# Optimization experiments

Measured on AMD Instinct MI355X. Metric: run time of the kernel, lower is better.

## Reference

```python
import jax, jax.numpy as jnp
import numpy as np

K, R, A, F, T = 100000, 5, 8, 32, 96
ROTATION_DELTA = 1


def setup_inputs() -> dict:
    key = jax.random.key(0)
    k1, k2, k3, k4, k5, k6, k7 = jax.random.split(key, 7)
    # barycentric coordinates: last dim packs (vertex_index, weight)
    idx = jax.random.randint(k1, (K, R, A, 3), 0, K)
    w = jax.random.uniform(k2, (K, R, A, 3), dtype=jnp.float32)
    w = w / jnp.sum(w, axis=-1, keepdims=True)
    bary_coordinates = jnp.stack([idx.astype(jnp.float32), w], axis=-1)  # (K,R,A,3,2)
    mesh_signal = jax.random.normal(k3, (K, F), dtype=jnp.float32)
    # kernel from define_kernel_values (abstract): fixed prior interpolation weights (R,A,R,A)
    kernel = jax.random.normal(k4, (R, A, R, A), dtype=jnp.float32) * 0.1
    template_neighbor_weights = jax.random.normal(k5, (T, R, A, F), dtype=jnp.float32) * 0.05
    template_self_weights = jax.random.normal(k6, (T, 1, F), dtype=jnp.float32) * 0.05
    bias = jax.random.normal(k7, (T,), dtype=jnp.float32) * 0.01
    return {
        "mesh_signal": mesh_signal,
        "bary_coordinates": bary_coordinates,
        "kernel": kernel,
        "template_neighbor_weights": template_neighbor_weights,
        "template_self_weights": template_self_weights,
        "bias": bias,
    }


def reference(mesh_signal, bary_coordinates, kernel, template_neighbor_weights,
              template_self_weights, bias):
    # --- signal retrieval: barycentric gather + interpolation ---
    idx = bary_coordinates[..., 0].astype(jnp.int32)          # (K,R,A,3)
    bw = bary_coordinates[..., 1]                              # (K,R,A,3)
    gathered = mesh_signal[idx]                                # (K,R,A,3,F)
    interp = jnp.sum(bw[..., None] * gathered, axis=-2)        # (K,R,A,F)
    # --- prior kernel fold (include_prior=True) ---
    interp = jnp.einsum('raxy,kxyf->kraf', kernel, interp)     # (K,R,A,F)
    # --- center contribution ---
    conv_center = jnp.einsum('tef,kf->ket', template_self_weights, mesh_signal)  # (K,1,T)
    # --- per-rotation template fold (torch.range is end-inclusive -> A//delta + 1 rotations) ---
    orientations = list(range(0, A + 1, ROTATION_DELTA))
    conv_neighbor = jnp.stack(
        [jnp.einsum('traf,kraf->kt', template_neighbor_weights,
                    jnp.roll(interp, o, axis=2)) + bias
         for o in orientations],
        axis=1)                                                # (K,O,T)
    return jax.nn.relu(conv_center + conv_neighbor)            # (K,O,T)
```

## Files before the change

### kernel.cpp

```cpp
#include <hip/hip_runtime.h>
#include <hip/hip_bf16.h>
#include <stdint.h>


typedef __attribute__((ext_vector_type(8))) short short8;
typedef __attribute__((ext_vector_type(4))) short short4v;
typedef __attribute__((ext_vector_type(4))) float floatx4;
typedef __attribute__((ext_vector_type(2))) float fx2;

#define KPTS 100000
#define OUT_STRIDE 864
#define BM 64
#define THREADS 512

#define BARRIER() do {                              \
    __builtin_amdgcn_sched_barrier(0);              \
    asm volatile("s_waitcnt lgkmcnt(0)");           \
    __builtin_amdgcn_s_barrier();                   \
  } while (0)

__device__ __forceinline__ short f2bf(float x) {
  union { float f; uint32_t u; } c; c.f = x;
  uint32_t u = c.u;
  u += 0x7FFFu + ((u >> 16) & 1u);
  return (short)(u >> 16);
}

__global__ void prep_B(const float* __restrict__ kern,
                       const float* __restrict__ tw,
                       const float* __restrict__ sw,
                       short* __restrict__ Bp) {
  const int ntile = blockIdx.x;
  const int ch    = blockIdx.y;
  const int lane  = threadIdx.x;
  const int n = ntile * 16 + (lane & 15);
  const int o = n / 96;
  const int t = n - o * 96;
  const int fb = (lane >> 4) * 8;

  short8 v;
  if (ch < 40) {
    float kcol[40];
#pragma unroll
    for (int ra = 0; ra < 40; ++ra) kcol[ra] = kern[ra * 40 + ch];
#pragma unroll
    for (int j = 0; j < 8; ++j) {
      const int f = fb + j;
      float acc = 0.f;
      for (int r = 0; r < 5; ++r) {
#pragma unroll
        for (int a = 0; a < 8; ++a) {
          acc += kcol[r * 8 + a] * tw[((t * 5 + r) * 8 + ((a + o) & 7)) * 32 + f];
        }
      }
      v[j] = f2bf(acc);
    }
  } else {
#pragma unroll
    for (int j = 0; j < 8; ++j) v[j] = f2bf(sw[t * 32 + fb + j]);
  }
  *reinterpret_cast<short8*>(Bp + ((size_t)(ch * 48 + ntile) * 64 + lane) * 8) = v;
}

__global__ __launch_bounds__(THREADS, 1) void conv_main(
    const float* __restrict__ ms,
    const float* __restrict__ bary,
    const float* __restrict__ bias,
    const short* __restrict__ Bp,
    float* __restrict__ out) {
  __shared__ short Atile[2][BM][40];

  const int kbase = blockIdx.x * BM;
  const int tid = threadIdx.x;
  const int lane = tid & 63;
  const int wn = tid >> 6;
  const int l15 = lane & 15;
  const int kh = lane >> 4;

  const int arow = tid >> 3;
  const int af0 = (tid & 7) * 4;
  const int krow = kbase + arow;
  const bool rowok = krow < KPTS;
  const float* __restrict__ brow = bary + (size_t)(rowok ? krow : 0) * 240;

  fx2 bE0, bE1, bE2, bO0, bO1, bO2;
  floatx4 eG0, eG1, eG2, oG0, oG1, oG2;
  float eW0, eW1, eW2, oW0, oW1, oW2;

  auto ldbary = [&](int c, fx2& p0, fx2& p1, fx2& p2) {
    if (rowok) {
      const fx2* bp = (const fx2*)(brow + c * 6);
      p0 = __builtin_nontemporal_load(bp);
      p1 = __builtin_nontemporal_load(bp + 1);
      p2 = __builtin_nontemporal_load(bp + 2);
    } else {
      p0 = (fx2)0.f; p1 = (fx2)0.f; p2 = (fx2)0.f;
    }
  };
  auto issueG = [&](int c, const fx2& p0, const fx2& p1, const fx2& p2,
                    floatx4& A, floatx4& B, floatx4& C,
                    float& W0, float& W1, float& W2) {
    if (c == 40) {
      A = *(const floatx4*)(ms + (size_t)(rowok ? krow : 0) * 32 + af0);
      B = (floatx4)0.f; C = (floatx4)0.f;
      W0 = rowok ? 1.f : 0.f; W1 = 0.f; W2 = 0.f;
    } else {
      A = *(const floatx4*)(ms + ((size_t)(int)p0.x) * 32 + af0);
      B = *(const floatx4*)(ms + ((size_t)(int)p1.x) * 32 + af0);
      C = *(const floatx4*)(ms + ((size_t)(int)p2.x) * 32 + af0);
      W0 = p0.y; W1 = p1.y; W2 = p2.y;
    }
  };
  auto commitG = [&](const floatx4& A, const floatx4& B, const floatx4& C,
                     float W0, float W1, float W2, int buf) {
    short4v s;
    s[0] = f2bf(W0 * A[0] + W1 * B[0] + W2 * C[0]);
    s[1] = f2bf(W0 * A[1] + W1 * B[1] + W2 * C[1]);
    s[2] = f2bf(W0 * A[2] + W1 * B[2] + W2 * C[2]);
    s[3] = f2bf(W0 * A[3] + W1 * B[3] + W2 * C[3]);
    *reinterpret_cast<short4v*>(&Atile[buf][arow][af0]) = s;
  };

  short8 bfA[6], bfB[6];
  auto loadB = [&](int c, short8* dst) {
    const short* bp = Bp + ((size_t)(c * 48 + wn * 6) * 64 + lane) * 8;
#pragma unroll
    for (int j = 0; j < 6; ++j)
      dst[j] = *reinterpret_cast<const short8*>(bp + (size_t)j * 512);
  };

  floatx4 acc[4][6];
#pragma unroll
  for (int mi = 0; mi < 4; ++mi)
#pragma unroll
    for (int nj = 0; nj < 6; ++nj) acc[mi][nj] = (floatx4)0.f;

  {
    fx2 t0, t1, t2;
    ldbary(0, t0, t1, t2);
    issueG(0, t0, t1, t2, eG0, eG1, eG2, eW0, eW1, eW2);
    ldbary(1, t0, t1, t2);
    issueG(1, t0, t1, t2, oG0, oG1, oG2, oW0, oW1, oW2);
  }
  ldbary(2, bE0, bE1, bE2);
  commitG(eG0, eG1, eG2, eW0, eW1, eW2, 0);
  loadB(0, bfA);
  BARRIER();

#define ITER(ch, UB0, UB1, UB2, FB0, FB1, FB2,                                  \
             FG0, FG1, FG2, FW0, FW1, FW2,                                      \
             CG0, CG1, CG2, CW0, CW1, CW2, CUR, BF, NBF)                        \
  {                                                                             \
    if ((ch) + 2 <= 40)                                                         \
      issueG((ch) + 2, UB0, UB1, UB2, FG0, FG1, FG2, FW0, FW1, FW2);            \
    if ((ch) + 3 <= 39) ldbary((ch) + 3, FB0, FB1, FB2);                        \
    short8 af[4];                                                               \
    _Pragma("unroll")                                                           \
    for (int mi = 0; mi < 4; ++mi)                                              \
      af[mi] = *reinterpret_cast<const short8*>(&Atile[CUR][mi * 16 + l15][kh * 8]); \
    if ((ch) + 1 <= 40) loadB((ch) + 1, NBF);                                   \
    _Pragma("unroll")                                                           \
    for (int nj = 0; nj < 6; ++nj)                                              \
      _Pragma("unroll")                                                         \
      for (int mi = 0; mi < 4; ++mi)                                            \
        acc[mi][nj] = __builtin_amdgcn_mfma_f32_16x16x32_bf16(af[mi], BF[nj],   \
                                                              acc[mi][nj], 0, 0, 0); \
    if ((ch) + 1 <= 40)                                                         \
      commitG(CG0, CG1, CG2, CW0, CW1, CW2, (CUR) ^ 1);                         \
    BARRIER();                                                                  \
  }

  for (int ch = 0; ch < 40; ch += 2) {
    ITER(ch,     bE0, bE1, bE2, bO0, bO1, bO2,
         eG0, eG1, eG2, eW0, eW1, eW2,
         oG0, oG1, oG2, oW0, oW1, oW2, 0, bfA, bfB)
    ITER(ch + 1, bO0, bO1, bO2, bE0, bE1, bE2,
         oG0, oG1, oG2, oW0, oW1, oW2,
         eG0, eG1, eG2, eW0, eW1, eW2, 1, bfB, bfA)
  }
  ITER(40, bE0, bE1, bE2, bO0, bO1, bO2,
       eG0, eG1, eG2, eW0, eW1, eW2,
       oG0, oG1, oG2, oW0, oW1, oW2, 0, bfA, bfB)
#undef ITER

#pragma unroll
  for (int mi = 0; mi < 4; ++mi) {
    const int rb = kbase + mi * 16 + kh * 4;
#pragma unroll
    for (int nj = 0; nj < 6; ++nj) {
      const int n = wn * 96 + nj * 16 + l15;
      const float bsv = bias[nj * 16 + l15];
      const bool dup = (wn == 0);
#pragma unroll
      for (int i = 0; i < 4; ++i) {
        const int r = rb + i;
        if (r < KPTS) {
          float vv = fmaxf(acc[mi][nj][i] + bsv, 0.f);
          out[(size_t)r * OUT_STRIDE + n] = vv;
          if (dup) out[(size_t)r * OUT_STRIDE + 768 + n] = vv;
        }
      }
    }
  }
}

extern "C" void kernel_launch(void* const* d_in, const int* in_sizes, int n_in,
                              void* d_out, int out_size, void* d_ws, size_t ws_size,
                              hipStream_t stream) {
  const float* ms   = (const float*)d_in[0];
  const float* bary = (const float*)d_in[1];
  const float* kern = (const float*)d_in[2];
  const float* tw   = (const float*)d_in[3];
  const float* sw   = (const float*)d_in[4];
  const float* bias = (const float*)d_in[5];
  float* out = (float*)d_out;
  short* Bp = (short*)d_ws;

  hipLaunchKernelGGL(prep_B, dim3(48, 41), dim3(64), 0, stream, kern, tw, sw, Bp);
  hipLaunchKernelGGL(conv_main, dim3(1563), dim3(THREADS), 0, stream,
                     ms, bary, bias, Bp, out);
}
```

Before: 453.9 us.

## Pre-convert mesh signal to bf16 and halve the gather threads

Adds a prep kernel that converts mesh_signal to bf16 in the workspace, so the random-row gathers in the main kernel fetch 16-byte short8 chunks instead of fp32 float4. Only half the threads (256) now build the A tile, each handling 8 features, while all threads still run the MFMAs. The aim is to halve gather bandwidth and the number of outstanding loads. The cost is an extra launch plus a full read and write of the signal, and the signal is rounded to bf16 before interpolation rather than after, which adds a little error.

```diff
diff --git a/kernel.cpp b/kernel.cpp
--- a/kernel.cpp
+++ b/kernel.cpp
@@ -4,7 +4,6 @@
 
 
 typedef __attribute__((ext_vector_type(8))) short short8;
-typedef __attribute__((ext_vector_type(4))) short short4v;
 typedef __attribute__((ext_vector_type(4))) float floatx4;
 typedef __attribute__((ext_vector_type(2))) float fx2;
 
@@ -12,6 +11,7 @@
 #define OUT_STRIDE 864
 #define BM 64
 #define THREADS 512
+#define BP_SHORTS 1007616
 
 #define BARRIER() do {                              \
     __builtin_amdgcn_sched_barrier(0);              \
@@ -24,6 +24,23 @@
   uint32_t u = c.u;
   u += 0x7FFFu + ((u >> 16) & 1u);
   return (short)(u >> 16);
+}
+__device__ __forceinline__ float bf2f(short s) {
+  union { uint32_t u; float f; } c;
+  c.u = ((uint32_t)(uint16_t)s) << 16;
+  return c.f;
+}
+
+__global__ void prep_ms(const float* __restrict__ ms, short* __restrict__ msb) {
+  const int i = (blockIdx.x * 256 + threadIdx.x) * 8;
+  if (i < KPTS * 32) {
+    floatx4 a = *(const floatx4*)(ms + i);
+    floatx4 b = *(const floatx4*)(ms + i + 4);
+    short8 s;
+#pragma unroll
+    for (int j = 0; j < 4; ++j) { s[j] = f2bf(a[j]); s[4 + j] = f2bf(b[j]); }
+    *reinterpret_cast<short8*>(msb + i) = s;
+  }
 }
 
 __global__ void prep_B(const float* __restrict__ kern,
@@ -63,7 +80,7 @@
 }
 
 __global__ __launch_bounds__(THREADS, 1) void conv_main(
-    const float* __restrict__ ms,
+    const short* __restrict__ msb,
     const float* __restrict__ bary,
     const float* __restrict__ bias,
     const short* __restrict__ Bp,
@@ -77,14 +94,16 @@
   const int l15 = lane & 15;
   const int kh = lane >> 4;
 
-  const int arow = tid >> 3;
-  const int af0 = (tid & 7) * 4;
-  const int krow = kbase + arow;
-  const bool rowok = krow < KPTS;
+  const bool builder = tid < 256;
+  const int arow = tid >> 2;
+  const int af0 = (tid & 3) * 8;
+  const int krow = kbase + (arow & 63);
+  const bool rowok = builder && (krow < KPTS);
   const float* __restrict__ brow = bary + (size_t)(rowok ? krow : 0) * 240;
+  const short* __restrict__ mrowb = msb + (size_t)(rowok ? krow : 0) * 32 + af0;
 
   fx2 bE0, bE1, bE2, bO0, bO1, bO2;
-  floatx4 eG0, eG1, eG2, oG0, oG1, oG2;
+  short8 eG0, eG1, eG2, oG0, oG1, oG2;
   float eW0, eW1, eW2, oW0, oW1, oW2;
 
   auto ldbary = [&](int c, fx2& p0, fx2& p1, fx2& p2) {
@@ -98,27 +117,26 @@
     }
   };
   auto issueG = [&](int c, const fx2& p0, const fx2& p1, const fx2& p2,
-                    floatx4& A, floatx4& B, floatx4& C,
+                    short8& A, short8& B, short8& C,
                     float& W0, float& W1, float& W2) {
     if (c == 40) {
-      A = *(const floatx4*)(ms + (size_t)(rowok ? krow : 0) * 32 + af0);
-      B = (floatx4)0.f; C = (floatx4)0.f;
+      A = *(const short8*)(mrowb);
+      B = A; C = A;
       W0 = rowok ? 1.f : 0.f; W1 = 0.f; W2 = 0.f;
     } else {
-      A = *(const floatx4*)(ms + ((size_t)(int)p0.x) * 32 + af0);
-      B = *(const floatx4*)(ms + ((size_t)(int)p1.x) * 32 + af0);
-      C = *(const floatx4*)(ms + ((size_t)(int)p2.x) * 32 + af0);
+      A = *(const short8*)(msb + ((size_t)(int)p0.x) * 32 + af0);
+      B = *(const short8*)(msb + ((size_t)(int)p1.x) * 32 + af0);
+      C = *(const short8*)(msb + ((size_t)(int)p2.x) * 32 + af0);
       W0 = p0.y; W1 = p1.y; W2 = p2.y;
     }
   };
-  auto commitG = [&](const floatx4& A, const floatx4& B, const floatx4& C,
+  auto commitG = [&](const short8& A, const short8& B, const short8& C,
                      float W0, float W1, float W2, int buf) {
-    short4v s;
-    s[0] = f2bf(W0 * A[0] + W1 * B[0] + W2 * C[0]);
-    s[1] = f2bf(W0 * A[1] + W1 * B[1] + W2 * C[1]);
-    s[2] = f2bf(W0 * A[2] + W1 * B[2] + W2 * C[2]);
-    s[3] = f2bf(W0 * A[3] + W1 * B[3] + W2 * C[3]);
-    *reinterpret_cast<short4v*>(&Atile[buf][arow][af0]) = s;
+    short8 s;
+#pragma unroll
+    for (int j = 0; j < 8; ++j)
+      s[j] = f2bf(W0 * bf2f(A[j]) + W1 * bf2f(B[j]) + W2 * bf2f(C[j]));
+    *reinterpret_cast<short8*>(&Atile[buf][arow][af0]) = s;
   };
 
   short8 bfA[6], bfB[6];
@@ -135,15 +153,15 @@
 #pragma unroll
     for (int nj = 0; nj < 6; ++nj) acc[mi][nj] = (floatx4)0.f;
 
-  {
+  if (builder) {
     fx2 t0, t1, t2;
     ldbary(0, t0, t1, t2);
     issueG(0, t0, t1, t2, eG0, eG1, eG2, eW0, eW1, eW2);
     ldbary(1, t0, t1, t2);
     issueG(1, t0, t1, t2, oG0, oG1, oG2, oW0, oW1, oW2);
-  }
-  ldbary(2, bE0, bE1, bE2);
-  commitG(eG0, eG1, eG2, eW0, eW1, eW2, 0);
+    ldbary(2, bE0, bE1, bE2);
+    commitG(eG0, eG1, eG2, eW0, eW1, eW2, 0);
+  }
   loadB(0, bfA);
   BARRIER();
 
@@ -151,9 +169,11 @@
              FG0, FG1, FG2, FW0, FW1, FW2,                                      \
              CG0, CG1, CG2, CW0, CW1, CW2, CUR, BF, NBF)                        \
   {                                                                             \
-    if ((ch) + 2 <= 40)                                                         \
-      issueG((ch) + 2, UB0, UB1, UB2, FG0, FG1, FG2, FW0, FW1, FW2);            \
-    if ((ch) + 3 <= 39) ldbary((ch) + 3, FB0, FB1, FB2);                        \
+    if (builder) {                                                              \
+      if ((ch) + 2 <= 40)                                                       \
+        issueG((ch) + 2, UB0, UB1, UB2, FG0, FG1, FG2, FW0, FW1, FW2);          \
+      if ((ch) + 3 <= 39) ldbary((ch) + 3, FB0, FB1, FB2);                      \
+    }                                                                           \
     short8 af[4];                                                               \
     _Pragma("unroll")                                                           \
     for (int mi = 0; mi < 4; ++mi)                                              \
@@ -165,7 +185,7 @@
       for (int mi = 0; mi < 4; ++mi)                                            \
         acc[mi][nj] = __builtin_amdgcn_mfma_f32_16x16x32_bf16(af[mi], BF[nj],   \
                                                               acc[mi][nj], 0, 0, 0); \
-    if ((ch) + 1 <= 40)                                                         \
+    if (builder && (ch) + 1 <= 40)                                              \
       commitG(CG0, CG1, CG2, CW0, CW1, CW2, (CUR) ^ 1);                         \
     BARRIER();                                                                  \
   }
@@ -214,9 +234,12 @@
   const float* sw   = (const float*)d_in[4];
   const float* bias = (const float*)d_in[5];
   float* out = (float*)d_out;
-  short* Bp = (short*)d_ws;
+  short* Bp  = (short*)d_ws;
+  short* msb = (short*)d_ws + BP_SHORTS;
 
   hipLaunchKernelGGL(prep_B, dim3(48, 41), dim3(64), 0, stream, kern, tw, sw, Bp);
+  hipLaunchKernelGGL(prep_ms, dim3((KPTS * 32 / 8 + 255) / 256), dim3(256), 0, stream,
+                     ms, msb);
   hipLaunchKernelGGL(conv_main, dim3(1563), dim3(THREADS), 0, stream,
-                     ms, bary, bias, Bp, out);
-}
+                     msb, bary, bias, Bp, out);
+}
```

Result: slower. 483.2 us (+6.5%).
